# Performance work log

Hardware: AMD Instinct MI355X
Metric: run time of the kernel (lower is better)

## Reference

```python
import jax, jax.numpy as jnp
import numpy as np

D_MODEL = 1024
N_HEADS = 16


def setup_inputs() -> dict:
    key = jax.random.key(0)
    ks = jax.random.split(key, 5)
    b, t, d = 4, 2048, D_MODEL
    x = jax.random.normal(ks[0], (b, t, d), dtype=jnp.float32)
    s = 1.0 / np.sqrt(d)
    qkv_w = jax.random.normal(ks[1], (d, 3 * d), dtype=jnp.float32) * s
    qkv_b = jnp.zeros((3 * d,), dtype=jnp.float32)
    o_w = jax.random.normal(ks[2], (d, d), dtype=jnp.float32) * s
    o_b = jnp.zeros((d,), dtype=jnp.float32)
    return {"x": x, "qkv_w": qkv_w, "qkv_b": qkv_b, "o_w": o_w, "o_b": o_b}


def reference(x, qkv_w, qkv_b, o_w, o_b):
    b, t, d = x.shape
    h = N_HEADS
    hd = d // h
    qkv = x @ qkv_w + qkv_b  # [b, t, 3d]
    q, k, v = jnp.split(qkv, 3, axis=-1)
    # [b, h, t, hd]
    q = q.reshape(b, t, h, hd).transpose(0, 2, 1, 3)
    k = k.reshape(b, t, h, hd).transpose(0, 2, 1, 3)
    v = v.reshape(b, t, h, hd).transpose(0, 2, 1, 3)
    scores = jnp.einsum("bhqd,bhkd->bhqk", q, k) / jnp.sqrt(jnp.float32(hd))
    causal = jnp.tril(jnp.ones((t, t), dtype=bool))
    scores = jnp.where(causal[None, None, :, :], scores, -jnp.inf)
    wts = jax.nn.softmax(scores, axis=-1)  # dropout p=0.0 -> identity
    y = jnp.einsum("bhqk,bhkd->bhqd", wts, v)
    y = y.transpose(0, 2, 1, 3).reshape(b, t, d)
    return y @ o_w + o_b
```

## Files before the change

kernel.cpp:

```cpp
#include <hip/hip_runtime.h>

typedef unsigned short ushort_t;
typedef __attribute__((ext_vector_type(8))) short short8;
typedef __attribute__((ext_vector_type(4))) float f32x4;
typedef __attribute__((ext_vector_type(4))) unsigned int uint4v;

__device__ __forceinline__ ushort_t f2bf(float f) {
  union { float f; unsigned int u; } v; v.f = f;
  unsigned int u = v.u;
  unsigned int r = (u + 0x7fffu + ((u >> 16) & 1u)) >> 16;
  return (ushort_t)r;
}

__device__ __forceinline__ unsigned int pk2(float hi, float lo) {
  union { float f; unsigned int u; } a, b; a.f = lo; b.f = hi;
  return __builtin_amdgcn_perm(b.u, a.u, 0x07060302u);
}

__device__ __forceinline__ void load_lds16(const void* g, void* l) {
  __builtin_amdgcn_global_load_lds(
      (const __attribute__((address_space(1))) unsigned int*)g,
      (__attribute__((address_space(3))) unsigned int*)l, 16, 0, 0);
}

__global__ __launch_bounds__(256) void prep(
    const float* __restrict__ x, ushort_t* __restrict__ Xb,
    const float* __restrict__ qkv_w, ushort_t* __restrict__ W1t,
    const float* __restrict__ o_w, ushort_t* __restrict__ W2t) {
  __shared__ float tile[64][65];
  const int blk = blockIdx.x;
  const int tid = threadIdx.x;
  if (blk < 4096) {
    int i = blk * 256 + tid;
    const float4* p = (const float4*)x;
    float4 a = p[2 * i];
    float4 b = p[2 * i + 1];
    short8 v;
    v[0] = (short)f2bf(a.x); v[1] = (short)f2bf(a.y);
    v[2] = (short)f2bf(a.z); v[3] = (short)f2bf(a.w);
    v[4] = (short)f2bf(b.x); v[5] = (short)f2bf(b.y);
    v[6] = (short)f2bf(b.z); v[7] = (short)f2bf(b.w);
    *(short8*)(Xb + (size_t)i * 8) = v;
    return;
  }
  const float* in;
  ushort_t* out;
  int R = 1024, C, c0, r0;
  if (blk < 4864) {
    int bx = blk - 4096;
    in = qkv_w; out = W1t; C = 3072;
    c0 = (bx % 48) * 64; r0 = (bx / 48) * 64;
  } else {
    int bx = blk - 4864;
    in = o_w; out = W2t; C = 1024;
    c0 = (bx % 16) * 64; r0 = (bx / 16) * 64;
  }
  for (int it = 0; it < 16; ++it) {
    int l = it * 256 + tid;
    int r = l >> 6, c = l & 63;
    tile[r][c] = in[(size_t)(r0 + r) * C + c0 + c];
  }
  __syncthreads();
  for (int it = 0; it < 16; ++it) {
    int l = it * 256 + tid;
    int ro = l >> 6, co = l & 63;
    out[(size_t)(c0 + ro) * R + r0 + co] = f2bf(tile[co][ro]);
  }
}

__device__ __forceinline__ void gemm_bt_main(
    const ushort_t* __restrict__ A, const ushort_t* __restrict__ Bt,
    int K, int bm, int bn, ushort_t* lds, f32x4 acc[4][4]) {
  const int tid = threadIdx.x;
  const int wave = tid >> 6, lane = tid & 63;
  const int quad = lane >> 4, col = lane & 15;
  const int wm = (wave & 1) * 64, wn = (wave >> 1) * 64;
  ushort_t* ldsA = lds;
  ushort_t* ldsB = lds + 8192;
  f32x4 z = {0.f, 0.f, 0.f, 0.f};
  for (int i = 0; i < 4; ++i)
    for (int j = 0; j < 4; ++j) acc[i][j] = z;
  for (int bk = 0; bk < K; bk += 64) {
    for (int is = 0; is < 4; ++is) {
      int o = is * 4096 + wave * 1024 + lane * 16;
      int p = o >> 13;
      int w = o & 8191;
      int r = w >> 6, kk = (w & 63) >> 1;
      int ldso = (is * 4096 + wave * 1024) >> 1;
      const ushort_t* ga = A + (size_t)(bm + r) * K + bk + p * 32 + kk;
      load_lds16(ga, ldsA + ldso);
      const ushort_t* gb = Bt + (size_t)(bn + r) * K + bk + p * 32 + kk;
      load_lds16(gb, ldsB + ldso);
    }
    __syncthreads();
    for (int ks = 0; ks < 2; ++ks) {
      short8 af[4], bfr[4];
      for (int i = 0; i < 4; ++i)
        af[i] = *(const short8*)(ldsA + ks * 4096 + (wm + i * 16 + col) * 32 + quad * 8);
      for (int j = 0; j < 4; ++j)
        bfr[j] = *(const short8*)(ldsB + ks * 4096 + (wn + j * 16 + col) * 32 + quad * 8);
      for (int i = 0; i < 4; ++i)
        for (int j = 0; j < 4; ++j)
          acc[i][j] = __builtin_amdgcn_mfma_f32_16x16x32_bf16(af[i], bfr[j], acc[i][j], 0, 0, 0);
    }
    __syncthreads();
  }
}

__global__ __launch_bounds__(512, 4) void gemm_qkv(
    const ushort_t* __restrict__ Xb, const ushort_t* __restrict__ W1t,
    const float* __restrict__ bias, ushort_t* __restrict__ Qb,
    ushort_t* __restrict__ Kb, ushort_t* __restrict__ Vtb) {
  __shared__ ushort_t lds[24576];
  const int K = 1024;
  const int bn = (blockIdx.x % 24) * 128;
  const int bm = (blockIdx.x / 24) * 256;
  const int tid = threadIdx.x;
  const int wave = tid >> 6, lane = tid & 63;
  const int quad = lane >> 4, col = lane & 15;
  const int wm = (wave & 3) * 64;
  const int wn = (wave >> 2) * 64;
  ushort_t* ldsA = lds;
  ushort_t* ldsB = lds + 16384;
  f32x4 z = {0.f, 0.f, 0.f, 0.f};
  f32x4 acc[4][4];
  for (int i = 0; i < 4; ++i)
    for (int j = 0; j < 4; ++j) acc[i][j] = z;

  for (int bk = 0; bk < K; bk += 64) {
#pragma unroll
    for (int is = 0; is < 4; ++is) {
      int o = is * 8192 + wave * 1024 + lane * 16;
      int p = o >> 14, w = o & 16383;
      int r = w >> 6, kk = (w & 63) >> 1;
      int ldso = (is * 8192 + wave * 1024) >> 1;
      load_lds16(Xb + (size_t)(bm + r) * K + bk + p * 32 + kk, ldsA + ldso);
    }
#pragma unroll
    for (int is = 0; is < 2; ++is) {
      int o = is * 8192 + wave * 1024 + lane * 16;
      int p = o >> 13, w = o & 8191;
      int r = w >> 6, kk = (w & 63) >> 1;
      int ldso = (is * 8192 + wave * 1024) >> 1;
      load_lds16(W1t + (size_t)(bn + r) * K + bk + p * 32 + kk, ldsB + ldso);
    }
    __syncthreads();
#pragma unroll
    for (int ks = 0; ks < 2; ++ks) {
      short8 af[4], bfr[4];
      for (int i = 0; i < 4; ++i)
        af[i] = *(const short8*)(ldsA + ks * 8192 + (wm + i * 16 + col) * 32 + quad * 8);
      for (int j = 0; j < 4; ++j)
        bfr[j] = *(const short8*)(ldsB + ks * 4096 + (wn + j * 16 + col) * 32 + quad * 8);
      for (int i = 0; i < 4; ++i)
        for (int j = 0; j < 4; ++j)
          acc[i][j] = __builtin_amdgcn_mfma_f32_16x16x32_bf16(af[i], bfr[j], acc[i][j], 0, 0, 0);
    }
    __syncthreads();
  }

  const float SCL = 0.18033688011112042f;
  const int which = bn >> 10;
  for (int i = 0; i < 4; ++i) {
    int row0 = bm + wm + i * 16 + quad * 4;
    int b = row0 >> 11, t0 = row0 & 2047;
    for (int j = 0; j < 4; ++j) {
      int cg = bn + wn + j * 16 + col;
      float bv = bias[cg];
      int rem = cg & 1023;
      int h = rem >> 6, hd = rem & 63;
      size_t bh = (size_t)(b * 16 + h);
      if (which == 0) {
        for (int r = 0; r < 4; ++r)
          Qb[(bh * 2048 + t0 + r) * 64 + hd] = f2bf((acc[i][j][r] + bv) * SCL);
      } else if (which == 1) {
        for (int r = 0; r < 4; ++r)
          Kb[(bh * 2048 + t0 + r) * 64 + hd] = f2bf(acc[i][j][r] + bv);
      } else {
        ushort4 pk;
        pk.x = f2bf(acc[i][j][0] + bv);
        pk.y = f2bf(acc[i][j][1] + bv);
        pk.z = f2bf(acc[i][j][2] + bv);
        pk.w = f2bf(acc[i][j][3] + bv);
        *(ushort4*)(Vtb + (bh * 64 + hd) * 2048 + t0) = pk;
      }
    }
  }
}

__global__ __launch_bounds__(256) void gemm_out_k(
    const ushort_t* __restrict__ Yb, const ushort_t* __restrict__ W2t,
    const float* __restrict__ bias, float* __restrict__ out) {
  __shared__ ushort_t lds[16384];
  const int ntile = 1024 / 128;
  int bn = (blockIdx.x % ntile) * 128;
  int bm = (blockIdx.x / ntile) * 128;
  f32x4 acc[4][4];
  gemm_bt_main(Yb, W2t, 1024, bm, bn, lds, acc);
  const int tid = threadIdx.x, wave = tid >> 6, lane = tid & 63;
  const int quad = lane >> 4, col = lane & 15;
  const int wm = (wave & 1) * 64, wn = (wave >> 1) * 64;
  for (int i = 0; i < 4; ++i) {
    int row0 = bm + wm + i * 16 + quad * 4;
    for (int j = 0; j < 4; ++j) {
      int cg = bn + wn + j * 16 + col;
      float bv = bias[cg];
      for (int r = 0; r < 4; ++r)
        out[(size_t)(row0 + r) * 1024 + cg] = acc[i][j][r] + bv;
    }
  }
}

#define KS_OFF 0
#define VS_OFF 9216
__global__ __launch_bounds__(256, 2) void attn(
    const ushort_t* __restrict__ Qb, const ushort_t* __restrict__ Kb,
    const ushort_t* __restrict__ Vtb, ushort_t* __restrict__ Yb) {
  __shared__ ushort_t lds[17920];
  const int tid = threadIdx.x, wave = tid >> 6, lane = tid & 63;
  const int quad = lane >> 4, col = lane & 15;
  const int bh = blockIdx.x & 63;
  const int a = blockIdx.x >> 6;
  const int b = bh >> 4, h = bh & 15;
  const ushort_t* Qg = Qb + (size_t)bh * 2048 * 64;
  const ushort_t* Kg = Kb + (size_t)bh * 2048 * 64;
  const ushort_t* Vg = Vtb + (size_t)bh * 64 * 2048;
  const int kv = tid;
  f32x4 z = {0.f, 0.f, 0.f, 0.f};

  for (int item = 0; item < 2; ++item) {
    const int qt = item == 0 ? 15 - a : a;
    const int q0 = qt * 128;
    short8 qf[2][2];
    for (int i = 0; i < 2; ++i)
      for (int ks = 0; ks < 2; ++ks)
        qf[i][ks] = *(const short8*)(
            Qg + (size_t)(q0 + wave * 32 + i * 16 + col) * 64 + ks * 32 + quad * 8);
    short8 kpre[4], vpre[4];
#pragma unroll
    for (int it = 0; it < 4; ++it) {
      int v = it * 256 + kv;
      kpre[it] = *(const short8*)(Kg + (size_t)(0 + (v >> 3)) * 64 + (v & 7) * 8);
      vpre[it] = *(const short8*)(Vg + (size_t)(v >> 4) * 2048 + 0 + (v & 15) * 8);
    }

    f32x4 oacc[2][4];
    float mst[2] = {-3.0e38f, -3.0e38f}, lst[2] = {0.f, 0.f};
    for (int i = 0; i < 2; ++i)
      for (int dt = 0; dt < 4; ++dt) oacc[i][dt] = z;

    for (int kt = 0; kt <= qt; ++kt) {
      int k0 = kt * 128;
      __syncthreads();
#pragma unroll
      for (int it = 0; it < 4; ++it) {
        int v = it * 256 + kv;
        *(short8*)(lds + KS_OFF + (v >> 3) * 72 + (v & 7) * 8) = kpre[it];
      }
#pragma unroll
      for (int it = 0; it < 4; ++it) {
        int v = it * 256 + kv;
        int d = v >> 4, kc = (v & 15) * 8;
        int p = kc >> 5, u = (kc >> 4) & 1, g0 = (kc >> 2) & 3;
        int pos1 = p * 32 + g0 * 8 + u * 4;
        short8 val = vpre[it];
        ushort4 lo4, hi4;
        lo4.x = (ushort_t)val[0]; lo4.y = (ushort_t)val[1];
        lo4.z = (ushort_t)val[2]; lo4.w = (ushort_t)val[3];
        hi4.x = (ushort_t)val[4]; hi4.y = (ushort_t)val[5];
        hi4.z = (ushort_t)val[6]; hi4.w = (ushort_t)val[7];
        *(ushort4*)(lds + VS_OFF + d * 136 + pos1) = lo4;
        *(ushort4*)(lds + VS_OFF + d * 136 + pos1 + 8) = hi4;
      }
      __syncthreads();
      if (kt < qt) {
        int k0n = k0 + 128;
#pragma unroll
        for (int it = 0; it < 4; ++it) {
          int v = it * 256 + kv;
          kpre[it] = *(const short8*)(Kg + (size_t)(k0n + (v >> 3)) * 64 + (v & 7) * 8);
          vpre[it] = *(const short8*)(Vg + (size_t)(v >> 4) * 2048 + k0n + (v & 15) * 8);
        }
      }
      f32x4 s[2][8];
      for (int i = 0; i < 2; ++i)
        for (int j = 0; j < 8; ++j) s[i][j] = z;
      for (int j = 0; j < 8; ++j) {
        short8 kf0 = *(const short8*)(lds + KS_OFF + (j * 16 + col) * 72 + quad * 8);
        short8 kf1 = *(const short8*)(lds + KS_OFF + (j * 16 + col) * 72 + 32 + quad * 8);
        for (int i = 0; i < 2; ++i) {
          s[i][j] = __builtin_amdgcn_mfma_f32_16x16x32_bf16(kf0, qf[i][0], s[i][j], 0, 0, 0);
          s[i][j] = __builtin_amdgcn_mfma_f32_16x16x32_bf16(kf1, qf[i][1], s[i][j], 0, 0, 0);
        }
      }
      if (kt == qt) {
        for (int i = 0; i < 2; ++i) {
          int qg = q0 + wave * 32 + i * 16 + col;
          for (int j = 0; j < 8; ++j) {
            int kg = k0 + j * 16 + quad * 4;
            for (int r = 0; r < 4; ++r)
              if (kg + r > qg) s[i][j][r] = -3.0e38f;
          }
        }
      }
      for (int i = 0; i < 2; ++i) {
        f32x4 vm = s[i][0];
        for (int j = 1; j < 8; ++j)
          for (int r = 0; r < 4; ++r) vm[r] = fmaxf(vm[r], s[i][j][r]);
        float rm = fmaxf(fmaxf(vm[0], vm[1]), fmaxf(vm[2], vm[3]));
        rm = fmaxf(rm, __shfl_xor(rm, 16));
        rm = fmaxf(rm, __shfl_xor(rm, 32));
        float mnew = fmaxf(mst[i], rm);
        float alpha = __builtin_amdgcn_exp2f(mst[i] - mnew);
        mst[i] = mnew;
        float rs = 0.f;
        for (int j = 0; j < 8; ++j)
          for (int r = 0; r < 4; ++r) {
            float p = __builtin_amdgcn_exp2f(s[i][j][r] - mnew);
            s[i][j][r] = p;
            rs += p;
          }
        rs += __shfl_xor(rs, 16);
        rs += __shfl_xor(rs, 32);
        lst[i] = lst[i] * alpha + rs;
        for (int dt = 0; dt < 4; ++dt)
          for (int r = 0; r < 4; ++r) oacc[i][dt][r] *= alpha;
      }
      for (int p2 = 0; p2 < 4; ++p2) {
        short8 pf[2];
        for (int i = 0; i < 2; ++i) {
          uint4v w;
          w[0] = pk2(s[i][2 * p2][1], s[i][2 * p2][0]);
          w[1] = pk2(s[i][2 * p2][3], s[i][2 * p2][2]);
          w[2] = pk2(s[i][2 * p2 + 1][1], s[i][2 * p2 + 1][0]);
          w[3] = pk2(s[i][2 * p2 + 1][3], s[i][2 * p2 + 1][2]);
          pf[i] = *(short8*)&w;
        }
        for (int dt = 0; dt < 4; ++dt) {
          short8 vf = *(const short8*)(lds + VS_OFF + (dt * 16 + col) * 136 + p2 * 32 + quad * 8);
          for (int i = 0; i < 2; ++i)
            oacc[i][dt] = __builtin_amdgcn_mfma_f32_16x16x32_bf16(vf, pf[i], oacc[i][dt], 0, 0, 0);
        }
      }
    }
    for (int i = 0; i < 2; ++i) {
      float linv = 1.0f / lst[i];
      int t = q0 + wave * 32 + i * 16 + col;
      size_t base = ((size_t)(b * 2048 + t)) * 1024 + h * 64;
      for (int dt = 0; dt < 4; ++dt) {
        ushort4 pk;
        pk.x = f2bf(oacc[i][dt][0] * linv);
        pk.y = f2bf(oacc[i][dt][1] * linv);
        pk.z = f2bf(oacc[i][dt][2] * linv);
        pk.w = f2bf(oacc[i][dt][3] * linv);
        *(ushort4*)(Yb + base + dt * 16 + quad * 4) = pk;
      }
    }
  }
}

extern "C" void kernel_launch(void* const* d_in, const int* in_sizes, int n_in,
                              void* d_out, int out_size, void* d_ws, size_t ws_size,
                              hipStream_t stream) {
  const float* x     = (const float*)d_in[0];
  const float* qkv_w = (const float*)d_in[1];
  const float* qkv_b = (const float*)d_in[2];
  const float* o_w   = (const float*)d_in[3];
  const float* o_b   = (const float*)d_in[4];
  float* out = (float*)d_out;
  char* ws = (char*)d_ws;
  ushort_t* Xb  = (ushort_t*)(ws);
  ushort_t* W1t = (ushort_t*)(ws + 16777216);
  ushort_t* W2t = (ushort_t*)(ws + 23068672);
  ushort_t* Qb  = (ushort_t*)(ws + 25165824);
  ushort_t* Kb  = (ushort_t*)(ws + 41943040);
  ushort_t* Vtb = (ushort_t*)(ws + 58720256);
  ushort_t* Yb  = Xb;

  prep<<<5120, 256, 0, stream>>>(x, Xb, qkv_w, W1t, o_w, W2t);
  gemm_qkv<<<768, 512, 0, stream>>>(Xb, W1t, qkv_b, Qb, Kb, Vtb);
  attn<<<512, 256, 0, stream>>>(Qb, Kb, Vtb, Yb);
  gemm_out_k<<<512, 256, 0, stream>>>(Yb, W2t, o_b, out);
}
```

Measured before the change: 245.0 us.

## Prefetch next QKV GEMM tile into registers to overlap loads with MFMA

The QKV projection GEMM no longer uses direct global-to-LDS loads issued right before a barrier. Instead it loads the next K-tile of X and W into registers while the current tile's MFMAs run, then stores the registers to LDS at the top of the next iteration. This hides global memory latency behind compute. The cost is extra VGPRs for the prefetch buffers and an extra register-to-LDS store pass, which could lower occupancy.

After: 235.4 us. 4.0% less time.

```diff
diff --git a/kernel.cpp b/kernel.cpp
--- a/kernel.cpp
+++ b/kernel.cpp
@@ -127,24 +127,51 @@
   for (int i = 0; i < 4; ++i)
     for (int j = 0; j < 4; ++j) acc[i][j] = z;
 
+  const ushort_t* aptr[4];
+  const ushort_t* bptr[2];
+  ushort_t* aslt[4];
+  ushort_t* bslt[2];
+#pragma unroll
+  for (int is = 0; is < 4; ++is) {
+    int o = is * 8192 + wave * 1024 + lane * 16;
+    int p = o >> 14, w = o & 16383;
+    int r = w >> 6, kk = (w & 63) >> 1;
+    aptr[is] = Xb + (size_t)(bm + r) * K + p * 32 + kk;
+    aslt[is] = ldsA + ((is * 8192 + wave * 1024) >> 1) + lane * 8;
+  }
+#pragma unroll
+  for (int is = 0; is < 2; ++is) {
+    int o = is * 8192 + wave * 1024 + lane * 16;
+    int p = o >> 13, w = o & 8191;
+    int r = w >> 6, kk = (w & 63) >> 1;
+    bptr[is] = W1t + (size_t)(bn + r) * K + p * 32 + kk;
+    bslt[is] = ldsB + ((is * 8192 + wave * 1024) >> 1) + lane * 8;
+  }
+  short8 apre[4], bpre[2];
+#pragma unroll
+  for (int is = 0; is < 4; ++is) apre[is] = *(const short8*)aptr[is];
+#pragma unroll
+  for (int is = 0; is < 2; ++is) bpre[is] = *(const short8*)bptr[is];
+
   for (int bk = 0; bk < K; bk += 64) {
-#pragma unroll
-    for (int is = 0; is < 4; ++is) {
-      int o = is * 8192 + wave * 1024 + lane * 16;
-      int p = o >> 14, w = o & 16383;
-      int r = w >> 6, kk = (w & 63) >> 1;
-      int ldso = (is * 8192 + wave * 1024) >> 1;
-      load_lds16(Xb + (size_t)(bm + r) * K + bk + p * 32 + kk, ldsA + ldso);
-    }
-#pragma unroll
-    for (int is = 0; is < 2; ++is) {
-      int o = is * 8192 + wave * 1024 + lane * 16;
-      int p = o >> 13, w = o & 8191;
-      int r = w >> 6, kk = (w & 63) >> 1;
-      int ldso = (is * 8192 + wave * 1024) >> 1;
-      load_lds16(W1t + (size_t)(bn + r) * K + bk + p * 32 + kk, ldsB + ldso);
-    }
     __syncthreads();
+#pragma unroll
+    for (int is = 0; is < 4; ++is) *(short8*)aslt[is] = apre[is];
+#pragma unroll
+    for (int is = 0; is < 2; ++is) *(short8*)bslt[is] = bpre[is];
+    __syncthreads();
+    if (bk + 64 < K) {
+#pragma unroll
+      for (int is = 0; is < 4; ++is) {
+        aptr[is] += 64;
+        apre[is] = *(const short8*)aptr[is];
+      }
+#pragma unroll
+      for (int is = 0; is < 2; ++is) {
+        bptr[is] += 64;
+        bpre[is] = *(const short8*)bptr[is];
+      }
+    }
 #pragma unroll
     for (int ks = 0; ks < 2; ++ks) {
       short8 af[4], bfr[4];
@@ -156,7 +183,6 @@
         for (int j = 0; j < 4; ++j)
           acc[i][j] = __builtin_amdgcn_mfma_f32_16x16x32_bf16(af[i], bfr[j], acc[i][j], 0, 0, 0);
     }
-    __syncthreads();
   }
 
   const float SCL = 0.18033688011112042f;
```
